# Performance work log

Hardware: AMD Instinct MI355X
Metric: run time of the kernel (lower is better)

Reference implementation:

```python
import jax, jax.numpy as jnp
import numpy as np
from jax import lax

QMIN, QMAX = -127, 127  # symmetric int8 range matching lut randint(-127,128)


def setup_inputs() -> dict:
    key = jax.random.key(0)
    k1, k2, k3, k4 = jax.random.split(key, 4)
    x = jax.random.normal(k1, (8, 3, 128, 128), jnp.float32)
    weight = jax.random.normal(k2, (16, 3, 3, 3), jnp.float32) * 0.1
    bias = jax.random.normal(k3, (16,), jnp.float32) * 0.01
    scale_x = jnp.float32(0.05)   # trainable per-tensor activation scale
    scale_w = jnp.float32(0.005)  # trainable per-tensor weight scale
    # LUT: row (a+128)*256 + (b+128) holds the approximate product of int8 a,b
    # as two int8 bytes (hi, lo); torch stores int8, we keep values in int32.
    lut = jax.random.randint(k4, (256 * 256, 2), -127, 128, jnp.int32)
    return {"x": x, "weight": weight, "bias": bias,
            "scale_x": scale_x, "scale_w": scale_w, "lut": lut}


def _lut_products(lut):
    # combine (hi, lo) int8 bytes into a 16-bit product value, [65536]
    hi = lut[:, 0].astype(jnp.int32)
    lo = lut[:, 1].astype(jnp.int32) & 255  # low byte is unsigned
    return hi * 256 + lo


def _approx_conv_int(qx, qw, lut):
    # qx: [B,Cin,H,W] int32 in [-127,127]; qw: [O,Cin,K,K] int32
    O = qw.shape[0]
    F = qw.shape[1] * qw.shape[2] * qw.shape[3]
    # im2col: [B, Cin*K*K, H, W], feature dim ordered (Cin, kh, kw)
    patches = lax.conv_general_dilated_patches(
        qx.astype(jnp.float32), (3, 3), (1, 1), ((1, 1), (1, 1))
    ).astype(jnp.int32)
    ip = patches + 128                      # [B, F, H, W], in [1,255]
    iw = qw.reshape(O, F) + 128             # [O, F]
    idx = ip[:, None] * 256 + iw[None, :, :, None, None]  # [B,O,F,H,W]
    prod = _lut_products(lut)[idx]          # gathered approx products, int32
    return prod.sum(axis=2)                 # [B, O, H, W] int32 accumulator


def reference(x, weight, bias, scale_x, scale_w, lut):
    # per-tensor int8 quantization
    qx = jnp.clip(jnp.round(x / scale_x), QMIN, QMAX).astype(jnp.int32)
    qw = jnp.clip(jnp.round(weight / scale_w), QMIN, QMAX).astype(jnp.int32)
    acc = _approx_conv_int(qx, qw, lut)     # LUT-approximated int conv
    out = acc.astype(jnp.float32) * (scale_x * scale_w)
    return out + bias[None, :, None, None]
```

## Files before the change

kernel.cpp:

```cpp
#include <hip/hip_runtime.h>

#define B_   8
#define CIN  3
#define OC   16
#define HH   128
#define WW   128
#define KK   3
#define FF   27
#define NSITE (B_*HH*WW)
#define OGRP 4
#define NCOL (OGRP*FF)
#define MBLK 512

__global__ void prep_kernel(const float* __restrict__ x,
                            const float* __restrict__ wgt,
                            const float* __restrict__ sx_p,
                            const float* __restrict__ sw_p,
                            const int*   __restrict__ lut,
                            short*       __restrict__ T,
                            int*         __restrict__ qwb,
                            unsigned char* __restrict__ qa)
{
    int i = blockIdx.x * blockDim.x + threadIdx.x;

    if (i < 65536) {
        int b = i >> 8, a = i & 255;
        int r = (a << 8) | b;
        int hi = lut[2 * r];
        int lo = lut[2 * r + 1] & 255;
        T[i] = (short)(hi * 256 + lo);
    }
    if (i < B_ * CIN * HH * WW) {
        float q = rintf(x[i] / sx_p[0]);
        q = fminf(127.f, fmaxf(-127.f, q));
        qa[i] = (unsigned char)((int)q + 128);
    }
    if (i < OC * FF) {
        float q = rintf(wgt[i] / sw_p[0]);
        q = fminf(127.f, fmaxf(-127.f, q));
        qwb[i] = (int)q + 128;
    }
}

__global__ __launch_bounds__(MBLK, 4) void conv_kernel(
    const unsigned char* __restrict__ qa,
    const int*   __restrict__ qwb,
    const short* __restrict__ T,
    const float* __restrict__ bias,
    const float* __restrict__ sx_p,
    const float* __restrict__ sw_p,
    float*       __restrict__ out)
{
    __shared__ short col[NCOL * 256];

    const int og   = blockIdx.x & 3;
    const int sblk = blockIdx.x >> 2;

    for (int e = threadIdx.x; e < NCOL * 256; e += MBLK) {
        int j  = e >> 8;
        int a  = e & 255;
        int ol = j / FF;
        int f  = j - ol * FF;
        int o  = og * OGRP + ol;
        col[e] = T[(qwb[o * FF + f] << 8) | a];
    }
    __syncthreads();

    const int s  = sblk * MBLK + threadIdx.x;
    const int b  = s >> 14;
    const int hw = s & 16383;
    const int h  = hw >> 7;
    const int w  = hw & 127;

    int av[FF];
    #pragma unroll
    for (int c = 0; c < CIN; ++c) {
        const unsigned char* base = qa + (b * CIN + c) * (HH * WW);
        #pragma unroll
        for (int kh = 0; kh < KK; ++kh) {
            int hh2 = h + kh - 1;
            #pragma unroll
            for (int kw = 0; kw < KK; ++kw) {
                int ww2 = w + kw - 1;
                int a = 128;
                if ((unsigned)hh2 < HH && (unsigned)ww2 < WW)
                    a = base[hh2 * WW + ww2];
                av[c * 9 + kh * 3 + kw] = a;
            }
        }
    }

    const float sxw = sx_p[0] * sw_p[0];
    #pragma unroll
    for (int ol = 0; ol < OGRP; ++ol) {
        int acc = 0;
        #pragma unroll
        for (int f = 0; f < FF; ++f) {
            acc += col[(ol * FF + f) * 256 + av[f]];
        }
        int o = og * OGRP + ol;
        out[((b * OC + o) * HH + h) * WW + w] = (float)acc * sxw + bias[o];
    }
}

extern "C" void kernel_launch(void* const* d_in, const int* in_sizes, int n_in,
                              void* d_out, int out_size, void* d_ws, size_t ws_size,
                              hipStream_t stream)
{
    const float* x    = (const float*)d_in[0];
    const float* wgt  = (const float*)d_in[1];
    const float* bias = (const float*)d_in[2];
    const float* sx   = (const float*)d_in[3];
    const float* sw   = (const float*)d_in[4];
    const int*   lut  = (const int*)d_in[5];

    char* ws = (char*)d_ws;
    short* T           = (short*)ws;
    int* qwb           = (int*)(ws + 131072);
    unsigned char* qa  = (unsigned char*)(ws + 131072 + 2048);

    prep_kernel<<<(B_ * CIN * HH * WW) / 256, 256, 0, stream>>>(
        x, wgt, sx, sw, lut, T, qwb, qa);

    conv_kernel<<<(NSITE / MBLK) * 4, MBLK, 0, stream>>>(
        qa, qwb, T, bias, sx, sw, (float*)d_out);
}
```

Before: 85.71 us.

## Pack four output-channel LUT products per entry and pad quantized input planes

The prep kernel now builds a weight-specialized table in which each (feature, activation) entry holds the four int16 products for a group of four output channels. The conv kernel can then fill shared memory with a straight int4 copy and do one 8-byte LDS read per feature instead of four 2-byte reads. The quantized input is stored with a one-pixel halo (130x130 planes), which removes the bounds checks from the im2col gather. The cost is a larger prep pass: it now does the 4-way LUT gathers per entry and writes padded planes.

```diff
diff --git a/kernel.cpp b/kernel.cpp
--- a/kernel.cpp
+++ b/kernel.cpp
@@ -1,68 +1,91 @@
 #include <hip/hip_runtime.h>
 
-#define B_   8
-#define CIN  3
-#define OC   16
-#define HH   128
-#define WW   128
-#define KK   3
-#define FF   27
+#define B_    8
+#define CIN   3
+#define OC    16
+#define HH    128
+#define WW    128
+#define KK    3
+#define FF    27
 #define NSITE (B_*HH*WW)
-#define OGRP 4
-#define NCOL (OGRP*FF)
-#define MBLK 512
+#define OGRP  4
+#define NGRP  (OC/OGRP)
+#define MBLK  512
+#define PH    130
+#define PLANE (PH*PH)
+#define QA_BYTES (B_*CIN*PLANE)
+#define T4_BYTES (NGRP*FF*256*4*2)
+#define SLAB_INT4 (FF*256*4*2/16)
 
 __global__ void prep_kernel(const float* __restrict__ x,
                             const float* __restrict__ wgt,
                             const float* __restrict__ sx_p,
                             const float* __restrict__ sw_p,
                             const int*   __restrict__ lut,
-                            short*       __restrict__ T,
-                            int*         __restrict__ qwb,
+                            short*       __restrict__ T4,
                             unsigned char* __restrict__ qa)
 {
-    int i = blockIdx.x * blockDim.x + threadIdx.x;
+    const int i = blockIdx.x * blockDim.x + threadIdx.x;
 
-    if (i < 65536) {
-        int b = i >> 8, a = i & 255;
-        int r = (a << 8) | b;
-        int hi = lut[2 * r];
-        int lo = lut[2 * r + 1] & 255;
-        T[i] = (short)(hi * 256 + lo);
+    if (i < B_ * CIN * PLANE) {
+        int bc = i / PLANE;
+        int p  = i - bc * PLANE;
+        int hp = p / PH;
+        int wp = p - hp * PH;
+        int h  = hp - 1;
+        int w  = wp - 1;
+        unsigned char v = 128;
+        if ((unsigned)h < HH && (unsigned)w < WW) {
+            float q = rintf(x[(bc * HH + h) * WW + w] / sx_p[0]);
+            q = fminf(127.f, fmaxf(-127.f, q));
+            v = (unsigned char)((int)q + 128);
+        }
+        qa[i] = v;
     }
-    if (i < B_ * CIN * HH * WW) {
-        float q = rintf(x[i] / sx_p[0]);
-        q = fminf(127.f, fmaxf(-127.f, q));
-        qa[i] = (unsigned char)((int)q + 128);
-    }
-    if (i < OC * FF) {
-        float q = rintf(wgt[i] / sw_p[0]);
-        q = fminf(127.f, fmaxf(-127.f, q));
-        qwb[i] = (int)q + 128;
+
+    if (i < NGRP * FF * 256) {
+        int og = i / (FF * 256);
+        int r  = i - og * (FF * 256);
+        int f  = r >> 8;
+        int a  = r & 255;
+        int vals[4];
+        #pragma unroll
+        for (int ol = 0; ol < 4; ++ol) {
+            int o = og * OGRP + ol;
+            float q = rintf(wgt[o * FF + f] / sw_p[0]);
+            q = fminf(127.f, fmaxf(-127.f, q));
+            int iw  = (int)q + 128;
+            int row = (a << 8) | iw;
+            int hi  = lut[2 * row];
+            int lo  = lut[2 * row + 1] & 255;
+            vals[ol] = hi * 256 + lo;
+        }
+        int2 d;
+        d.x = (vals[1] << 16) | (vals[0] & 0xffff);
+        d.y = (vals[3] << 16) | (vals[2] & 0xffff);
+        *reinterpret_cast<int2*>(T4 + (size_t)i * 4) = d;
     }
 }
 
 __global__ __launch_bounds__(MBLK, 4) void conv_kernel(
     const unsigned char* __restrict__ qa,
-    const int*   __restrict__ qwb,
-    const short* __restrict__ T,
+    const short* __restrict__ T4,
     const float* __restrict__ bias,
     const float* __restrict__ sx_p,
     const float* __restrict__ sw_p,
     float*       __restrict__ out)
 {
-    __shared__ short col[NCOL * 256];
+    __shared__ int2 colv[FF * 256];
 
     const int og   = blockIdx.x & 3;
     const int sblk = blockIdx.x >> 2;
 
-    for (int e = threadIdx.x; e < NCOL * 256; e += MBLK) {
-        int j  = e >> 8;
-        int a  = e & 255;
-        int ol = j / FF;
-        int f  = j - ol * FF;
-        int o  = og * OGRP + ol;
-        col[e] = T[(qwb[o * FF + f] << 8) | a];
+    {
+        const int4* __restrict__ src =
+            reinterpret_cast<const int4*>(T4 + (size_t)og * FF * 256 * 4);
+        int4* dst = reinterpret_cast<int4*>(colv);
+        for (int c = threadIdx.x; c < SLAB_INT4; c += MBLK)
+            dst[c] = src[c];
     }
     __syncthreads();
 
@@ -75,32 +98,32 @@
     int av[FF];
     #pragma unroll
     for (int c = 0; c < CIN; ++c) {
-        const unsigned char* base = qa + (b * CIN + c) * (HH * WW);
+        const unsigned char* __restrict__ bp =
+            qa + (b * CIN + c) * PLANE + h * PH + w;
         #pragma unroll
-        for (int kh = 0; kh < KK; ++kh) {
-            int hh2 = h + kh - 1;
+        for (int kh = 0; kh < KK; ++kh)
             #pragma unroll
-            for (int kw = 0; kw < KK; ++kw) {
-                int ww2 = w + kw - 1;
-                int a = 128;
-                if ((unsigned)hh2 < HH && (unsigned)ww2 < WW)
-                    a = base[hh2 * WW + ww2];
-                av[c * 9 + kh * 3 + kw] = a;
-            }
-        }
+            for (int kw = 0; kw < KK; ++kw)
+                av[c * 9 + kh * 3 + kw] = bp[kh * PH + kw];
+    }
+
+    int acc0 = 0, acc1 = 0, acc2 = 0, acc3 = 0;
+    #pragma unroll
+    for (int f = 0; f < FF; ++f) {
+        int2 d = colv[f * 256 + av[f]];
+        acc0 += (short)d.x;
+        acc1 += d.x >> 16;
+        acc2 += (short)d.y;
+        acc3 += d.y >> 16;
     }
 
     const float sxw = sx_p[0] * sw_p[0];
-    #pragma unroll
-    for (int ol = 0; ol < OGRP; ++ol) {
-        int acc = 0;
-        #pragma unroll
-        for (int f = 0; f < FF; ++f) {
-            acc += col[(ol * FF + f) * 256 + av[f]];
-        }
-        int o = og * OGRP + ol;
-        out[((b * OC + o) * HH + h) * WW + w] = (float)acc * sxw + bias[o];
-    }
+    const int   ob  = og * OGRP;
+    float* op = out + ((b * OC + ob) * HH + h) * WW + w;
+    op[0 * HH * WW] = (float)acc0 * sxw + bias[ob + 0];
+    op[1 * HH * WW] = (float)acc1 * sxw + bias[ob + 1];
+    op[2 * HH * WW] = (float)acc2 * sxw + bias[ob + 2];
+    op[3 * HH * WW] = (float)acc3 * sxw + bias[ob + 3];
 }
 
 extern "C" void kernel_launch(void* const* d_in, const int* in_sizes, int n_in,
@@ -115,13 +138,12 @@
     const int*   lut  = (const int*)d_in[5];
 
     char* ws = (char*)d_ws;
-    short* T           = (short*)ws;
-    int* qwb           = (int*)(ws + 131072);
-    unsigned char* qa  = (unsigned char*)(ws + 131072 + 2048);
+    short*         T4 = (short*)ws;
+    unsigned char* qa = (unsigned char*)(ws + T4_BYTES);
 
-    prep_kernel<<<(B_ * CIN * HH * WW) / 256, 256, 0, stream>>>(
-        x, wgt, sx, sw, lut, T, qwb, qa);
+    prep_kernel<<<(B_ * CIN * PLANE + 255) / 256, 256, 0, stream>>>(
+        x, wgt, sx, sw, lut, T4, qa);
 
-    conv_kernel<<<(NSITE / MBLK) * 4, MBLK, 0, stream>>>(
-        qa, qwb, T, bias, sx, sw, (float*)d_out);
+    conv_kernel<<<(NSITE / MBLK) * NGRP, MBLK, 0, stream>>>(
+        qa, T4, bias, sx, sw, (float*)d_out);
 }
```

Result: faster. 76.24 us (-11.0%).
